# Optimization experiments

Measured on AMD Instinct MI355X. Metric: run time of the kernel, lower is better.

Reference implementation:

```python
import math
import jax, jax.numpy as jnp
import numpy as np

B = 2
N = 48           # max_atoms
A = 16           # num_atom_types
E = 5            # num_bond_types
HID = 384
NH = 8
HD = HID // NH   # 48
LYR = 4
MLP = 4 * HID
L = N + N * N    # 2352 sequence length (nodes + flattened edges)


def setup_inputs() -> dict:
    key = jax.random.key(0)
    ks = iter(jax.random.split(key, 48))
    r = lambda *s: jax.random.normal(next(ks), s, jnp.float32) * 0.02
    d = {
        "x": jax.random.normal(next(ks), (B, N, A), jnp.float32),
        "adj": jax.random.normal(next(ks), (B, N, N, E), jnp.float32),
        "t": jax.random.uniform(next(ks), (B,), jnp.float32),
        # embeddings
        "node_w": r(A, HID), "node_b": jnp.zeros((HID,), jnp.float32),
        "edge_w": r(E, HID), "edge_b": jnp.zeros((HID,), jnp.float32),
        "pos": r(L, HID),
        # timestep MLP (SinusoidalPositionalEmbedding(HID) -> Linear(HID,4H) -> SiLU -> Linear(4H,H))
        "t_w1": r(HID, 4 * HID), "t_b1": jnp.zeros((4 * HID,), jnp.float32),
        "t_w2": r(4 * HID, HID), "t_b2": jnp.zeros((HID,), jnp.float32),
        # stacked per-layer params
        "ada1_w": r(LYR, HID, 2 * HID), "ada1_b": jnp.zeros((LYR, 2 * HID), jnp.float32),
        "ada2_w": r(LYR, HID, 2 * HID), "ada2_b": jnp.zeros((LYR, 2 * HID), jnp.float32),
        "q_w": r(LYR, HID, HID), "q_b": jnp.zeros((LYR, HID), jnp.float32),
        "k_w": r(LYR, HID, HID), "k_b": jnp.zeros((LYR, HID), jnp.float32),
        "v_w": r(LYR, HID, HID), "v_b": jnp.zeros((LYR, HID), jnp.float32),
        "o_w": r(LYR, HID, HID), "o_b": jnp.zeros((LYR, HID), jnp.float32),
        "m1_w": r(LYR, HID, MLP), "m1_b": jnp.zeros((LYR, MLP), jnp.float32),
        "m2_w": r(LYR, MLP, HID), "m2_b": jnp.zeros((LYR, HID), jnp.float32),
        # final norm + heads (heads random instead of zero-init so output is informative)
        "fn_g": jnp.ones((HID,), jnp.float32), "fn_b": jnp.zeros((HID,), jnp.float32),
        "on_w": r(HID, A), "on_b": jnp.zeros((A,), jnp.float32),
        "oe_w": r(HID, E), "oe_b": jnp.zeros((E,), jnp.float32),
    }
    return d


def _ln(z):
    # LayerNorm(elementwise_affine=False), eps=1e-5
    mu = z.mean(-1, keepdims=True)
    var = z.var(-1, keepdims=True)
    return (z - mu) * jax.lax.rsqrt(var + 1e-5)


def _forward(x, adj, t, node_w, node_b, edge_w, edge_b, pos,
             t_w1, t_b1, t_w2, t_b2,
             ada1_w, ada1_b, ada2_w, ada2_b,
             q_w, q_b, k_w, k_b, v_w, v_b, o_w, o_b,
             m1_w, m1_b, m2_w, m2_b,
             fn_g, fn_b, on_w, on_b, oe_w, oe_b):
    b = x.shape[0]
    # embed nodes and edges, concat into sequence [b, L, HID]
    h_nodes = x @ node_w + node_b                       # [b, N, H]
    h_edges = adj.reshape(b, N * N, E) @ edge_w + edge_b  # [b, N*N, H]
    h = jnp.concatenate([h_nodes, h_edges], axis=1) + pos[None]
    # sinusoidal timestep embedding -> cond [b, HID]
    half = HID // 2
    freqs = jnp.exp(-math.log(10000.0) * jnp.arange(half, dtype=jnp.float32) / half)
    ang = t[:, None].astype(jnp.float32) * freqs[None, :]
    temb = jnp.concatenate([jnp.sin(ang), jnp.cos(ang)], axis=-1)
    cond = jax.nn.silu(temb @ t_w1 + t_b1) @ t_w2 + t_b2
    inv_scale = 1.0 / math.sqrt(HD)
    for i in range(LYR):
        # AdaLN 1 + attention
        sc, sh = jnp.split(cond @ ada1_w[i] + ada1_b[i], 2, axis=-1)
        n = _ln(h) * (1.0 + sc[:, None, :]) + sh[:, None, :]
        q = (n @ q_w[i] + q_b[i]).reshape(b, L, NH, HD)
        k = (n @ k_w[i] + k_b[i]).reshape(b, L, NH, HD)
        v = (n @ v_w[i] + v_b[i]).reshape(b, L, NH, HD)
        scores = jnp.einsum('bqhd,bkhd->bhqk', q, k) * inv_scale
        attn = jax.nn.softmax(scores, axis=-1)
        ao = jnp.einsum('bhqk,bkhd->bqhd', attn, v).reshape(b, L, HID)
        h = h + ao @ o_w[i] + o_b[i]
        # AdaLN 2 + MLP (exact GELU as in nn.GELU default)
        sc2, sh2 = jnp.split(cond @ ada2_w[i] + ada2_b[i], 2, axis=-1)
        n2 = _ln(h) * (1.0 + sc2[:, None, :]) + sh2[:, None, :]
        h = h + jax.nn.gelu(n2 @ m1_w[i] + m1_b[i], approximate=False) @ m2_w[i] + m2_b[i]
    h = _ln(h) * fn_g + fn_b
    node_out = h[:, :N] @ on_w + on_b                   # [b, N, A]
    edge_out = (h[:, N:] @ oe_w + oe_b).reshape(b, N, N, E)
    return node_out, edge_out


def reference(x, adj, t, node_w, node_b, edge_w, edge_b, pos,
              t_w1, t_b1, t_w2, t_b2,
              ada1_w, ada1_b, ada2_w, ada2_b,
              q_w, q_b, k_w, k_b, v_w, v_b, o_w, o_b,
              m1_w, m1_b, m2_w, m2_b,
              fn_g, fn_b, on_w, on_b, oe_w, oe_b):
    return _forward(x, adj, t, node_w, node_b, edge_w, edge_b, pos,
                    t_w1, t_b1, t_w2, t_b2,
                    ada1_w, ada1_b, ada2_w, ada2_b,
                    q_w, q_b, k_w, k_b, v_w, v_b, o_w, o_b,
                    m1_w, m1_b, m2_w, m2_b,
                    fn_g, fn_b, on_w, on_b, oe_w, oe_b)
```

## Files before the change

### kernel.cpp

```cpp
#include <hip/hip_runtime.h>
#include <hip/hip_bf16.h>
#include <math.h>

typedef __hip_bfloat16 bf16;
typedef __attribute__((ext_vector_type(8))) short short8;
typedef __attribute__((ext_vector_type(4))) float f32x4;

#define B_ 2
#define N_ 48
#define A_ 16
#define E_ 5
#define HID 384
#define NHD 8
#define HD 48
#define LYR 4
#define MLPD 1536
#define L_ 2352
#define M_ 4704
#define VLP 2432
#define QSCALE 0.20823513f

#define WQ_  0LL
#define WK_  589824LL
#define WV_  1179648LL
#define WO_  1769472LL
#define WM1_ 2359296LL
#define WM2_ 4718592LL
#define WTOT 7077888
#define BQ_  0
#define BK_  1536
#define BV_  3072
#define BO_  4608
#define BM1_ 6144
#define BM2_ 12288
#define BTOT 13824

#define PO_E  ((size_t)16*2368*2*48)
#define PML_E ((size_t)16*2368*2*2)

#define GLOAD16(gp, lp) __builtin_amdgcn_global_load_lds( \
    (const __attribute__((address_space(1))) unsigned int*)(gp), \
    (__attribute__((address_space(3))) unsigned int*)(lp), 16, 0, 0)

static __device__ __forceinline__ float b2f(bf16 v) { return __bfloat162float(v); }
static __device__ __forceinline__ float us2f(unsigned short u) {
    return __uint_as_float(((unsigned)u) << 16);
}
static __device__ __forceinline__ unsigned short f2us(float f) {
    bf16 h = __float2bfloat16(f);
    return *reinterpret_cast<unsigned short*>(&h);
}
static __device__ __forceinline__ float exp2_raw(float x) {
    float r;
    asm("v_exp_f32 %0, %1" : "=v"(r) : "v"(x));
    return r;
}
static __device__ __forceinline__ float ldv(const float* p, size_t i) { return p[i]; }
static __device__ __forceinline__ float ldv(const bf16*  p, size_t i) { return b2f(p[i]); }
static __device__ __forceinline__ void  stv(float* p, size_t i, float v) { p[i] = v; }
static __device__ __forceinline__ void  stv(bf16*  p, size_t i, float v) { p[i] = __float2bfloat16(v); }
static __device__ __forceinline__ float4 ld4(const float* p, size_t i) {
    return *reinterpret_cast<const float4*>(p + i);
}
static __device__ __forceinline__ float4 ld4(const bf16* p, size_t i) {
    ushort4 u = *reinterpret_cast<const ushort4*>(p + i);
    return make_float4(us2f(u.x), us2f(u.y), us2f(u.z), us2f(u.w));
}

__global__ void k_detect(const void* w, int* flag) {
    if (threadIdx.x == 0 && blockIdx.x == 0) {
        const bf16* p = (const bf16*)w;
        int isf = 0;
        for (int i = 0; i < 256; ++i) {
            float v = fabsf(b2f(p[i]));
            if (!(v <= 1000.0f)) { isf = 1; break; }
        }
        *flag = isf;
    }
}

template <typename T>
static __device__ void prepw_body(
    const T* q_w, const T* k_w, const T* v_w, const T* o_w,
    const T* m1_w, const T* m2_w, bf16* wbt)
{
    __shared__ unsigned short Ts[64][72];
    const int z = blockIdx.y;
    const int kind = z >> 2, l = z & 3;
    const T* src; int K, N; long long dbase;
    switch (kind) {
        case 0: src = q_w;  K = 384;  N = 384;  dbase = WQ_;  break;
        case 1: src = k_w;  K = 384;  N = 384;  dbase = WK_;  break;
        case 2: src = v_w;  K = 384;  N = 384;  dbase = WV_;  break;
        case 3: src = o_w;  K = 384;  N = 384;  dbase = WO_;  break;
        case 4: src = m1_w; K = 384;  N = 1536; dbase = WM1_; break;
        default: src = m2_w; K = 1536; N = 384; dbase = WM2_; break;
    }
    const int Nt = N >> 6;
    const int tiles = (K >> 6) * Nt;
    if (blockIdx.x >= tiles) return;
    const int tk = blockIdx.x / Nt, tn = blockIdx.x % Nt;
    const int k0 = tk*64, n0 = tn*64;
    const size_t soff = (size_t)l * K * N;
    const size_t doff = (size_t)dbase + (size_t)l * K * N;
    const int tid = threadIdx.x;
    {
        const int kk = tid >> 2, nc = (tid & 3) * 16;
        #pragma unroll
        for (int j = 0; j < 16; ++j)
            Ts[kk][nc + j] = f2us(ldv(src, soff + (size_t)(k0 + kk)*N + n0 + nc + j));
    }
    __syncthreads();
    {
        const int nn = tid >> 2, kc = (tid & 3) * 16;
        unsigned short tmp[16];
        #pragma unroll
        for (int j = 0; j < 16; ++j) tmp[j] = Ts[kc + j][nn];
        unsigned short* dst = (unsigned short*)wbt + doff + (size_t)(n0 + nn)*K + k0 + kc;
        *reinterpret_cast<short8*>(dst)     = *reinterpret_cast<short8*>(&tmp[0]);
        *reinterpret_cast<short8*>(dst + 8) = *reinterpret_cast<short8*>(&tmp[8]);
    }
}

__global__ __launch_bounds__(256) void k_prepw(
    const void* q_w, const void* k_w, const void* v_w, const void* o_w,
    const void* m1_w, const void* m2_w, const int* __restrict__ fl, bf16* __restrict__ wbt)
{
    if (*fl) prepw_body<float>((const float*)q_w, (const float*)k_w, (const float*)v_w,
                               (const float*)o_w, (const float*)m1_w, (const float*)m2_w, wbt);
    else     prepw_body<bf16>((const bf16*)q_w, (const bf16*)k_w, (const bf16*)v_w,
                              (const bf16*)o_w, (const bf16*)m1_w, (const bf16*)m2_w, wbt);
}

template <typename T>
static __device__ void prepb_body(
    const T* q_b, const T* k_b, const T* v_b, const T* o_b,
    const T* m1_b, const T* m2_b, bf16* bb)
{
    for (int i = threadIdx.x; i < BTOT; i += 256) {
        float v;
        if      (i < BK_)  v = ldv(q_b,  i);
        else if (i < BV_)  v = ldv(k_b,  i - BK_);
        else if (i < BO_)  v = ldv(v_b,  i - BV_);
        else if (i < BM1_) v = ldv(o_b,  i - BO_);
        else if (i < BM2_) v = ldv(m1_b, i - BM1_);
        else               v = ldv(m2_b, i - BM2_);
        bb[i] = __float2bfloat16(v);
    }
}

__global__ __launch_bounds__(256) void k_prepb(
    const void* q_b, const void* k_b, const void* v_b, const void* o_b,
    const void* m1_b, const void* m2_b, const int* __restrict__ fl, bf16* __restrict__ bb)
{
    if (*fl) prepb_body<float>((const float*)q_b, (const float*)k_b, (const float*)v_b,
                               (const float*)o_b, (const float*)m1_b, (const float*)m2_b, bb);
    else     prepb_body<bf16>((const bf16*)q_b, (const bf16*)k_b, (const bf16*)v_b,
                              (const bf16*)o_b, (const bf16*)m1_b, (const bf16*)m2_b, bb);
}

template <typename T>
static __device__ void embed_body(
    const T* x, const T* adj, const T* node_w, const T* node_b,
    const T* edge_w, const T* edge_b, const T* pos, float* h)
{
    const int bl = blockIdx.x;
    const int b = bl / L_, l = bl % L_;
    const int c = threadIdx.x;
    float acc;
    if (l < N_) {
        acc = ldv(node_b, c);
        const size_t xr = (size_t)(b*N_ + l)*A_;
        #pragma unroll
        for (int a = 0; a < A_; ++a) acc += ldv(x, xr + a) * ldv(node_w, (size_t)a*HID + c);
    } else {
        const int e = l - N_;
        acc = ldv(edge_b, c);
        const size_t ar = ((size_t)b*N_*N_ + e)*E_;
        #pragma unroll
        for (int j = 0; j < E_; ++j) acc += ldv(adj, ar + j) * ldv(edge_w, (size_t)j*HID + c);
    }
    h[(size_t)bl*HID + c] = acc + ldv(pos, (size_t)l*HID + c);
}

__global__ __launch_bounds__(384) void k_embed(
    const void* x, const void* adj, const void* node_w, const void* node_b,
    const void* edge_w, const void* edge_b, const void* pos,
    const int* __restrict__ fl, float* __restrict__ h)
{
    if (*fl) embed_body<float>((const float*)x, (const float*)adj, (const float*)node_w,
                               (const float*)node_b, (const float*)edge_w, (const float*)edge_b,
                               (const float*)pos, h);
    else     embed_body<bf16>((const bf16*)x, (const bf16*)adj, (const bf16*)node_w,
                              (const bf16*)node_b, (const bf16*)edge_w, (const bf16*)edge_b,
                              (const bf16*)pos, h);
}

template <typename T>
static __device__ void cond1_body(const T* t, const T* t_w1, const T* t_b1, float* hid)
{
    __shared__ float temb[HID];
    __shared__ float red[4][64];
    const int b = blockIdx.x, jb = blockIdx.y, tid = threadIdx.x;
    const float tv = ldv(t, b);
    for (int c = tid; c < HID; c += 256) {
        int i = (c < 192) ? c : c - 192;
        float f = expf(-9.2103403719761836f * (float)i / 192.0f);
        float ang = tv * f;
        temb[c] = (c < 192) ? sinf(ang) : cosf(ang);
    }
    __syncthreads();
    const int ko = tid >> 6, jo = tid & 63;
    const int j = jb*64 + jo;
    float acc = 0.f;
    for (int i = ko*96; i < (ko + 1)*96; ++i)
        acc += temb[i] * ldv(t_w1, (size_t)i*4*HID + j);
    red[ko][jo] = acc;
    __syncthreads();
    if (ko == 0) {
        float a = red[0][jo] + red[1][jo] + red[2][jo] + red[3][jo] + ldv(t_b1, j);
        hid[(size_t)b*4*HID + j] = a / (1.0f + expf(-a));
    }
}

__global__ __launch_bounds__(256) void k_cond1(
    const void* t, const void* t_w1, const void* t_b1,
    const int* __restrict__ fl, float* __restrict__ hid)
{
    if (*fl) cond1_body<float>((const float*)t, (const float*)t_w1, (const float*)t_b1, hid);
    else     cond1_body<bf16>((const bf16*)t, (const bf16*)t_w1, (const bf16*)t_b1, hid);
}

template <typename T>
static __device__ void cond2_body(const T* t_w2, const T* t_b2, const float* hid, float* part)
{
    __shared__ float hs[128];
    const int b = blockIdx.x, ch = blockIdx.y, c = threadIdx.x;
    const int j0 = ch*128;
    if (c < 128) hs[c] = hid[(size_t)b*4*HID + j0 + c];
    __syncthreads();
    float acc = (ch == 0) ? ldv(t_b2, c) : 0.f;
    for (int jj = 0; jj < 128; ++jj)
        acc += hs[jj] * ldv(t_w2, (size_t)(j0 + jj)*HID + c);
    part[((size_t)b*12 + ch)*HID + c] = acc;
}

__global__ __launch_bounds__(384) void k_cond2(
    const void* t_w2, const void* t_b2, const int* __restrict__ fl,
    const float* __restrict__ hid, float* __restrict__ part)
{
    if (*fl) cond2_body<float>((const float*)t_w2, (const float*)t_b2, hid, part);
    else     cond2_body<bf16>((const bf16*)t_w2, (const bf16*)t_b2, hid, part);
}

template <typename T>
static __device__ void cond3_body(
    const T* ada1_w, const T* ada1_b, const T* ada2_w, const T* ada2_b,
    const float* part, float* ada_out)
{
    __shared__ float cs[HID];
    const int slot = blockIdx.x / 3, ob = blockIdx.x % 3, b = blockIdx.y;
    const int tid = threadIdx.x;
    for (int c = tid; c < HID; c += 256) {
        float s = 0.f;
        #pragma unroll
        for (int ch = 0; ch < 12; ++ch) s += part[((size_t)b*12 + ch)*HID + c];
        cs[c] = s;
    }
    __syncthreads();
    const int layer = slot >> 1, which = slot & 1;
    const int o = ob*256 + tid;
    const T* W  = which ? ada2_w : ada1_w;
    const T* Bi = which ? ada2_b : ada1_b;
    float acc = ldv(Bi, (size_t)layer*768 + o);
    const size_t wb = (size_t)layer*HID*768 + o;
    for (int c = 0; c < HID; ++c) acc += cs[c] * ldv(W, wb + (size_t)c*768);
    ada_out[((size_t)slot*B_ + b)*768 + o] = acc;
}

__global__ __launch_bounds__(256) void k_cond3(
    const void* ada1_w, const void* ada1_b, const void* ada2_w, const void* ada2_b,
    const int* __restrict__ fl, const float* __restrict__ part, float* __restrict__ ada_out)
{
    if (*fl) cond3_body<float>((const float*)ada1_w, (const float*)ada1_b,
                               (const float*)ada2_w, (const float*)ada2_b, part, ada_out);
    else     cond3_body<bf16>((const bf16*)ada1_w, (const bf16*)ada1_b,
                              (const bf16*)ada2_w, (const bf16*)ada2_b, part, ada_out);
}

__global__ __launch_bounds__(256) void k_adaln(
    const float* __restrict__ h, const float* __restrict__ ada,
    bf16* __restrict__ n, int slot)
{
    const int row  = blockIdx.x * 4 + (threadIdx.x >> 6);
    const int lane = threadIdx.x & 63;
    const int b = row / L_;
    const float* hr = h + (size_t)row*HID;
    float v[6]; float s = 0.f, ss = 0.f;
    #pragma unroll
    for (int j = 0; j < 6; ++j) { float t = hr[lane + j*64]; v[j] = t; s += t; ss += t*t; }
    #pragma unroll
    for (int off = 32; off; off >>= 1) { s += __shfl_xor(s, off); ss += __shfl_xor(ss, off); }
    const float mu = s * (1.0f/HID);
    const float rs = rsqrtf(fmaxf(ss * (1.0f/HID) - mu*mu, 0.0f) + 1e-5f);
    const float* ap = ada + ((size_t)slot*B_ + b)*768;
    bf16* nr = n + (size_t)row*HID;
    #pragma unroll
    for (int j = 0; j < 6; ++j) {
        int c = lane + j*64;
        nr[c] = __float2bfloat16((v[j] - mu)*rs*(1.0f + ap[c]) + ap[384 + c]);
    }
}

static __device__ __forceinline__ void gemm_epilogue(
    f32x4 (&acc)[2][2], float bcol0, float bcol1,
    bf16* Cb, float* Cf, int M, int N, int act, int mode,
    int bm, int bn, int wm, int wn, int quad, int c)
{
    const float bcol[2] = {bcol0, bcol1};
    #pragma unroll
    for (int mi = 0; mi < 2; ++mi)
        #pragma unroll
        for (int ni = 0; ni < 2; ++ni) {
            const int col = bn + wn*32 + ni*16 + c;
            #pragma unroll
            for (int r = 0; r < 4; ++r) {
                const int row = bm + wm*32 + mi*16 + quad*4 + r;
                if (row < M) {
                    float v = acc[mi][ni][r] + bcol[ni];
                    if (act) v = 0.5f * v * (1.0f + erff(v * 0.70710678118654752f));
                    if (mode == 1) Cf[(size_t)row*N + col] += v;
                    else if (mode == 0) Cb[(size_t)row*N + col] = __float2bfloat16(v);
                    else if (mode == 3) Cb[(size_t)row*N + col] = __float2bfloat16(v * QSCALE);
                    else {
                        const int b   = row >= L_ ? 1 : 0;
                        const int key = row - b*L_;
                        const int hh  = col / 48, d = col - hh*48;
                        Cb[((size_t)(b*8 + hh)*48 + d)*VLP + key] = __float2bfloat16(v);
                    }
                }
            }
        }
}

template <typename T>
static __device__ void gemm_body(
    const bf16* A, const T* W, long long woff, const T* bias, long long boff,
    bf16* Cb, float* Cf, int M, int N, int K, int act, int mode)
{
    __shared__ __align__(16) unsigned short As[64][72];
    __shared__ __align__(16) unsigned short Bt[64][72];
    const int tid  = threadIdx.x;
    const int wv   = tid >> 6, lane = tid & 63;
    const int quad = lane >> 4, c = lane & 15;
    const int wm = wv & 1, wn = wv >> 1;
    const int bm = blockIdx.x * 64, bn = blockIdx.y * 64;
    const int arow = tid >> 3, ach = tid & 7;
    f32x4 acc[2][2] = {{{0.f,0.f,0.f,0.f},{0.f,0.f,0.f,0.f}},
                       {{0.f,0.f,0.f,0.f},{0.f,0.f,0.f,0.f}}};
    for (int k0 = 0; k0 < K; k0 += 64) {
        short8 av[2]; float4 w0[2], w1[2];
        #pragma unroll
        for (int i = 0; i < 2; ++i) {
            const int row = i*32 + arow;
            av[i] = short8{0,0,0,0,0,0,0,0};
            if (bm + row < M)
                av[i] = *reinterpret_cast<const short8*>(
                            A + (size_t)(bm + row)*K + k0 + ach*8);
            const size_t wrow = (size_t)woff + (size_t)(k0 + i*32 + arow)*N + bn + ach*8;
            w0[i] = ld4(W, wrow);
            w1[i] = ld4(W, wrow + 4);
        }
        __syncthreads();
        #pragma unroll
        for (int i = 0; i < 2; ++i) {
            *reinterpret_cast<short8*>(&As[i*32 + arow][ach*8]) = av[i];
            const int kk = i*32 + arow, nb0 = ach*8;
            Bt[nb0+0][kk] = f2us(w0[i].x); Bt[nb0+1][kk] = f2us(w0[i].y);
            Bt[nb0+2][kk] = f2us(w0[i].z); Bt[nb0+3][kk] = f2us(w0[i].w);
            Bt[nb0+4][kk] = f2us(w1[i].x); Bt[nb0+5][kk] = f2us(w1[i].y);
            Bt[nb0+6][kk] = f2us(w1[i].z); Bt[nb0+7][kk] = f2us(w1[i].w);
        }
        __syncthreads();
        #pragma unroll
        for (int ks = 0; ks < 2; ++ks) {
            short8 af[2], bfr[2];
            #pragma unroll
            for (int mi = 0; mi < 2; ++mi)
                af[mi] = *reinterpret_cast<const short8*>(
                             &As[wm*32 + mi*16 + c][ks*32 + quad*8]);
            #pragma unroll
            for (int ni = 0; ni < 2; ++ni)
                bfr[ni] = *reinterpret_cast<const short8*>(
                              &Bt[wn*32 + ni*16 + c][ks*32 + quad*8]);
            #pragma unroll
            for (int mi = 0; mi < 2; ++mi)
                #pragma unroll
                for (int ni = 0; ni < 2; ++ni)
                    acc[mi][ni] = __builtin_amdgcn_mfma_f32_16x16x32_bf16(
                                      af[mi], bfr[ni], acc[mi][ni], 0, 0, 0);
        }
    }
    gemm_epilogue(acc, ldv(bias, (size_t)boff + bn + wn*32 + c),
                  ldv(bias, (size_t)boff + bn + wn*32 + 16 + c),
                  Cb, Cf, M, N, act, mode, bm, bn, wm, wn, quad, c);
}

__global__ __launch_bounds__(256) void k_gemm(
    const bf16* __restrict__ A, const void* W, long long woff, const void* bias, long long boff,
    bf16* Cb, float* Cf, int M, int N, int K, int act, int mode,
    const int* __restrict__ fl)
{
    if (*fl) gemm_body<float>(A, (const float*)W, woff, (const float*)bias, boff,
                              Cb, Cf, M, N, K, act, mode);
    else     gemm_body<bf16>(A, (const bf16*)W, woff, (const bf16*)bias, boff,
                             Cb, Cf, M, N, K, act, mode);
}

__global__ __launch_bounds__(256) void k_gemm_qkv(
    const bf16* __restrict__ A,
    const void* qw, const void* kw, const void* vw,
    const void* qb, const void* kb, const void* vb,
    long long woff, long long boff,
    bf16* Cq, bf16* Ck, bf16* Cv, const int* __restrict__ fl)
{
    const int z = blockIdx.z;
    const void* W  = (z == 0) ? qw : (z == 1) ? kw : vw;
    const void* Bi = (z == 0) ? qb : (z == 1) ? kb : vb;
    bf16* C        = (z == 0) ? Cq : (z == 1) ? Ck : Cv;
    const int mode = (z == 0) ? 3 : (z == 2) ? 2 : 0;
    if (*fl) gemm_body<float>(A, (const float*)W, woff, (const float*)Bi, boff,
                              C, nullptr, M_, HID, HID, 0, mode);
    else     gemm_body<bf16>(A, (const bf16*)W, woff, (const bf16*)Bi, boff,
                             C, nullptr, M_, HID, HID, 0, mode);
}

static __device__ void gemm_t_body(
    const bf16* A, const bf16* Wt, long long woff, const bf16* bias, long long boff,
    bf16* Cb, float* Cf, int M, int N, int K, int act, int mode)
{
    __shared__ __align__(16) unsigned short Tz[2][2][4096];
    const int tid  = threadIdx.x;
    const int wv   = tid >> 6, lane = tid & 63;
    const int quad = lane >> 4, c = lane & 15;
    const int wm = wv & 1, wn = wv >> 1;
    const int bm = blockIdx.x * 64, bn = blockIdx.y * 64;
    const unsigned short* Ag = (const unsigned short*)A;
    const unsigned short* Wg = (const unsigned short*)Wt + woff;
    const int sr = tid >> 3;
    const int csw0 = (((tid & 7) ^ (sr & 7)) << 3);
    int ar0 = bm + sr;        ar0 = ar0 < M ? ar0 : M - 1;
    int ar1 = bm + 32 + sr;   ar1 = ar1 < M ? ar1 : M - 1;
    const int wr0 = bn + sr, wr1 = bn + 32 + sr;
    const int ldso = tid * 8;

    f32x4 acc[2][2] = {{{0.f,0.f,0.f,0.f},{0.f,0.f,0.f,0.f}},
                       {{0.f,0.f,0.f,0.f},{0.f,0.f,0.f,0.f}}};

    #define STAGE_T(buf, k0) do { \
        GLOAD16(Ag + (size_t)ar0*K + (k0) + csw0, &Tz[buf][0][ldso]); \
        GLOAD16(Ag + (size_t)ar1*K + (k0) + csw0, &Tz[buf][0][2048 + ldso]); \
        GLOAD16(Wg + (size_t)wr0*K + (k0) + csw0, &Tz[buf][1][ldso]); \
        GLOAD16(Wg + (size_t)wr1*K + (k0) + csw0, &Tz[buf][1][2048 + ldso]); \
    } while (0)

    STAGE_T(0, 0);
    __syncthreads();
    int cur = 0;
    for (int k0 = 0; k0 < K; k0 += 64) {
        if (k0 + 64 < K) STAGE_T(cur ^ 1, k0 + 64);
        #pragma unroll
        for (int ks = 0; ks < 2; ++ks) {
            short8 af[2], bfr[2];
            #pragma unroll
            for (int mi = 0; mi < 2; ++mi) {
                const int row = wm*32 + mi*16 + c;
                const char* p = (const char*)&Tz[cur][0][0]
                              + (row*128 + (((ks*64 + quad*16)) ^ ((row & 7) << 4)));
                af[mi] = *reinterpret_cast<const short8*>(p);
            }
            #pragma unroll
            for (int ni = 0; ni < 2; ++ni) {
                const int row = wn*32 + ni*16 + c;
                const char* p = (const char*)&Tz[cur][1][0]
                              + (row*128 + (((ks*64 + quad*16)) ^ ((row & 7) << 4)));
                bfr[ni] = *reinterpret_cast<const short8*>(p);
            }
            #pragma unroll
            for (int mi = 0; mi < 2; ++mi)
                #pragma unroll
                for (int ni = 0; ni < 2; ++ni)
                    acc[mi][ni] = __builtin_amdgcn_mfma_f32_16x16x32_bf16(
                                      af[mi], bfr[ni], acc[mi][ni], 0, 0, 0);
        }
        __syncthreads();
        cur ^= 1;
    }
    #undef STAGE_T
    gemm_epilogue(acc, b2f(bias[boff + bn + wn*32 + c]),
                  b2f(bias[boff + bn + wn*32 + 16 + c]),
                  Cb, Cf, M, N, act, mode, bm, bn, wm, wn, quad, c);
}

__global__ __launch_bounds__(256) void k_gemm_t(
    const bf16* __restrict__ A, const bf16* __restrict__ Wt, long long woff,
    const bf16* __restrict__ bias, long long boff,
    bf16* Cb, float* Cf, int M, int N, int K, int act, int mode)
{
    gemm_t_body(A, Wt, woff, bias, boff, Cb, Cf, M, N, K, act, mode);
}

__global__ __launch_bounds__(256) void k_gemm_qkv_t(
    const bf16* __restrict__ A, const bf16* __restrict__ wbt, const bf16* __restrict__ bb,
    int lyr, bf16* Cq, bf16* Ck, bf16* Cv)
{
    const int z = blockIdx.z;
    long long woff; long long boff; bf16* C; int mode;
    if (z == 0)      { woff = WQ_ + (long long)lyr*147456; boff = BQ_ + lyr*384; C = Cq; mode = 3; }
    else if (z == 1) { woff = WK_ + (long long)lyr*147456; boff = BK_ + lyr*384; C = Ck; mode = 0; }
    else             { woff = WV_ + (long long)lyr*147456; boff = BV_ + lyr*384; C = Cv; mode = 2; }
    gemm_t_body(A, wbt, woff, bb, boff, C, nullptr, M_, HID, HID, 0, mode);
}

__global__ __launch_bounds__(512) void k_attn(
    const bf16* __restrict__ q, const bf16* __restrict__ k,
    const bf16* __restrict__ vt, bf16* __restrict__ ao)
{
    __shared__ __align__(16) unsigned short Ks[2][64][80];
    __shared__ __align__(16) unsigned short Vt[2][48][72];
    __shared__ __align__(16) unsigned short Pq[8][16][72];
    const int tid  = threadIdx.x;
    const int w    = tid >> 6, lane = tid & 63;
    const int quad = lane >> 4, c = lane & 15;
    const int qt = w & 3, sp = w >> 2;
    const int bh = blockIdx.y;
    const size_t base  = (size_t)(bh >> 3)*L_*HID + (size_t)(bh & 7)*HD;
    const size_t vbase = (size_t)bh*48*VLP;
    const int q0 = blockIdx.x*64 + qt*16;
    const bool qvalid = q0 < L_;
    const int qrow = qvalid ? (q0 + c) : c;

    short8 qf0, qf1;
    {
        const unsigned short* qp = (const unsigned short*)(q + base + (size_t)qrow*HID);
        qf0 = *reinterpret_cast<const short8*>(qp + quad*8);
        if (quad < 2) qf1 = *reinterpret_cast<const short8*>(qp + 32 + quad*8);
        else          qf1 = short8{0,0,0,0,0,0,0,0};
    }
    f32x4 o0 = {0.f,0.f,0.f,0.f}, o1 = {0.f,0.f,0.f,0.f}, o2 = {0.f,0.f,0.f,0.f};
    float m = -3.0e38f, lsum = 0.f;

    const int t256 = tid & 255, grp = tid >> 8;
    const int krow0 = t256 >> 3, kch = t256 & 7;
    const int krow1 = 32 + krow0;
    const int vd0 = krow0;
    const int vd1 = 32 + (krow0 & 15);
    const bool vl1 = (t256 < 128);
    const unsigned short* kq = (const unsigned short*)(k + base);
    const unsigned short* vq = (const unsigned short*)(vt + vbase);
    const short8 Z8 = short8{0,0,0,0,0,0,0,0};
    short8 kr0 = Z8, kr1 = Z8, vr0, vr1 = Z8;
    {
        const int kb0 = grp*1216;
        if (kch < 6) {
            kr0 = *reinterpret_cast<const short8*>(kq + (size_t)(kb0 + krow0)*HID + kch*8);
            kr1 = *reinterpret_cast<const short8*>(kq + (size_t)(kb0 + krow1)*HID + kch*8);
        }
        vr0 = *reinterpret_cast<const short8*>(vq + (size_t)vd0*VLP + kb0 + kch*8);
        if (vl1) vr1 = *reinterpret_cast<const short8*>(vq + (size_t)vd1*VLP + kb0 + kch*8);
    }

    for (int tt = 0; tt < 19; ++tt) {
        __syncthreads();
        *reinterpret_cast<short8*>(&Ks[grp][krow0][kch*8]) = kr0;
        *reinterpret_cast<short8*>(&Ks[grp][krow1][kch*8]) = kr1;
        *reinterpret_cast<short8*>(&Vt[grp][vd0][kch*8])   = vr0;
        if (vl1) *reinterpret_cast<short8*>(&Vt[grp][vd1][kch*8]) = vr1;
        __syncthreads();
        if (tt < 18) {
            const int nb0 = grp*1216 + (tt + 1)*64;
            if (kch < 6) {
                kr0 = *reinterpret_cast<const short8*>(kq + (size_t)(nb0 + krow0)*HID + kch*8);
                kr1 = *reinterpret_cast<const short8*>(kq + (size_t)(nb0 + krow1)*HID + kch*8);
            }
            vr0 = *reinterpret_cast<const short8*>(vq + (size_t)vd0*VLP + nb0 + kch*8);
            if (vl1) vr1 = *reinterpret_cast<const short8*>(vq + (size_t)vd1*VLP + nb0 + kch*8);
        }

        const int kt = sp*1216 + tt*64;
        float sv[16];
        #pragma unroll
        for (int t = 0; t < 4; ++t) {
            f32x4 acc = {0.f,0.f,0.f,0.f};
            short8 a0 = *reinterpret_cast<const short8*>(&Ks[sp][t*16 + c][quad*8]);
            short8 a1 = *reinterpret_cast<const short8*>(&Ks[sp][t*16 + c][32 + quad*8]);
            acc = __builtin_amdgcn_mfma_f32_16x16x32_bf16(a0, qf0, acc, 0, 0, 0);
            acc = __builtin_amdgcn_mfma_f32_16x16x32_bf16(a1, qf1, acc, 0, 0, 0);
            #pragma unroll
            for (int r = 0; r < 4; ++r) sv[t*4 + r] = acc[r];
        }
        if (sp == 1 && tt >= 17) {
            #pragma unroll
            for (int t = 0; t < 4; ++t)
                #pragma unroll
                for (int r = 0; r < 4; ++r)
                    if (kt + t*16 + quad*4 + r >= L_) sv[t*4 + r] = -3.0e38f;
        }
        float tmax = fmaxf(fmaxf(fmaxf(sv[0], sv[1]),  fmaxf(sv[2],  sv[3])),
                           fmaxf(fmaxf(sv[4], sv[5]),  fmaxf(sv[6],  sv[7])));
        float tmx2 = fmaxf(fmaxf(fmaxf(sv[8], sv[9]),  fmaxf(sv[10], sv[11])),
                           fmaxf(fmaxf(sv[12], sv[13]), fmaxf(sv[14], sv[15])));
        tmax = fmaxf(tmax, tmx2);
        tmax = fmaxf(tmax, __shfl_xor(tmax, 16));
        tmax = fmaxf(tmax, __shfl_xor(tmax, 32));
        if (!__all(tmax <= m + 8.0f)) {
            const float mn = fmaxf(m, tmax);
            const float alpha = exp2f(m - mn);
            m = mn;
            lsum *= alpha;
            o0 *= alpha; o1 *= alpha; o2 *= alpha;
        }
        float psum = 0.f;
        unsigned short pv[16];
        #pragma unroll
        for (int i = 0; i < 16; ++i) {
            const float p = exp2f(sv[i] - m);
            psum += p;
            pv[i] = f2us(p);
        }
        lsum += psum;
        #pragma unroll
        for (int t = 0; t < 4; ++t)
            *reinterpret_cast<ushort4*>(&Pq[w][c][t*16 + quad*4]) =
                make_ushort4(pv[t*4+0], pv[t*4+1], pv[t*4+2], pv[t*4+3]);
        #pragma unroll
        for (int s = 0; s < 2; ++s) {
            short8 pf  = *reinterpret_cast<const short8*>(&Pq[w][c][s*32 + quad*8]);
            short8 vf0 = *reinterpret_cast<const short8*>(&Vt[sp][c][s*32 + quad*8]);
            short8 vf1 = *reinterpret_cast<const short8*>(&Vt[sp][16 + c][s*32 + quad*8]);
            short8 vf2 = *reinterpret_cast<const short8*>(&Vt[sp][32 + c][s*32 + quad*8]);
            o0 = __builtin_amdgcn_mfma_f32_16x16x32_bf16(vf0, pf, o0, 0, 0, 0);
            o1 = __builtin_amdgcn_mfma_f32_16x16x32_bf16(vf1, pf, o1, 0, 0, 0);
            o2 = __builtin_amdgcn_mfma_f32_16x16x32_bf16(vf2, pf, o2, 0, 0, 0);
        }
    }
    float lw = lsum;
    lw += __shfl_xor(lw, 16);
    lw += __shfl_xor(lw, 32);
    float* Mg = (float*)&Ks[0][0][0];
    __syncthreads();
    if (sp == 1) {
        float* dst = Mg + (size_t)(qt*64 + lane)*14;
        dst[0] = o0[0]; dst[1] = o0[1]; dst[2]  = o0[2]; dst[3]  = o0[3];
        dst[4] = o1[0]; dst[5] = o1[1]; dst[6]  = o1[2]; dst[7]  = o1[3];
        dst[8] = o2[0]; dst[9] = o2[1]; dst[10] = o2[2]; dst[11] = o2[3];
        dst[12] = m; dst[13] = lw;
    }
    __syncthreads();
    if (sp == 0 && qvalid) {
        const float* src = Mg + (size_t)(qt*64 + lane)*14;
        const float m2 = src[12], l2 = src[13];
        const float mm = fmaxf(m, m2);
        const float a1 = exp2f(m - mm), a2 = exp2f(m2 - mm);
        const float inv = 1.0f / (lw*a1 + l2*a2);
        unsigned short* orow = (unsigned short*)(ao + base + (size_t)(q0 + c)*HID);
        const f32x4 ot[3] = {o0, o1, o2};
        #pragma unroll
        for (int dt = 0; dt < 3; ++dt) {
            ushort4 w4;
            w4.x = f2us((ot[dt][0]*a1 + src[dt*4+0]*a2) * inv);
            w4.y = f2us((ot[dt][1]*a1 + src[dt*4+1]*a2) * inv);
            w4.z = f2us((ot[dt][2]*a1 + src[dt*4+2]*a2) * inv);
            w4.w = f2us((ot[dt][3]*a1 + src[dt*4+3]*a2) * inv);
            *reinterpret_cast<ushort4*>(orow + dt*16 + quad*4) = w4;
        }
    }
}

__global__ __launch_bounds__(256) void k_attn_fd(
    const bf16* __restrict__ q, const bf16* __restrict__ k,
    const bf16* __restrict__ vt, bf16* __restrict__ pob, float* __restrict__ pml)
{
    __shared__ __align__(16) unsigned short Ks[64][80];
    __shared__ __align__(16) unsigned short Vt[48][72];
    __shared__ __align__(16) unsigned short Pq[4][16][72];
    const int tid  = threadIdx.x;
    const int w    = tid >> 6, lane = tid & 63;
    const int quad = lane >> 4, c = lane & 15;
    const int bh   = blockIdx.y;
    const int half = blockIdx.z;
    const size_t base  = (size_t)(bh >> 3)*L_*HID + (size_t)(bh & 7)*HD;
    const size_t vbase = (size_t)bh*48*VLP;
    const int q0 = blockIdx.x*64 + w*16;
    const bool qvalid = q0 < L_;
    const int qrow = qvalid ? (q0 + c) : c;

    short8 qf0, qf1;
    {
        const unsigned short* qp = (const unsigned short*)(q + base + (size_t)qrow*HID);
        qf0 = *reinterpret_cast<const short8*>(qp + quad*8);
        if (quad < 2) qf1 = *reinterpret_cast<const short8*>(qp + 32 + quad*8);
        else          qf1 = short8{0,0,0,0,0,0,0,0};
    }
    f32x4 o0 = {0.f,0.f,0.f,0.f}, o1 = {0.f,0.f,0.f,0.f}, o2 = {0.f,0.f,0.f,0.f};
    float m = -3.0e38f, lsum = 0.f;

    const int krow0 = tid >> 3, kch = tid & 7;
    const int krow1 = 32 + krow0;
    const int vd0 = krow0;
    const int vd1 = 32 + (krow0 & 15);
    const bool vl1 = (tid < 128);
    const unsigned short* kq = (const unsigned short*)(k + base);
    const unsigned short* vq = (const unsigned short*)(vt + vbase);
    const short8 Z8 = short8{0,0,0,0,0,0,0,0};
    short8 kr0 = Z8, kr1 = Z8, vr0, vr1 = Z8;
    const int kbase = half*1216;
    {
        if (kch < 6) {
            kr0 = *reinterpret_cast<const short8*>(kq + (size_t)(kbase + krow0)*HID + kch*8);
            kr1 = *reinterpret_cast<const short8*>(kq + (size_t)(kbase + krow1)*HID + kch*8);
        }
        vr0 = *reinterpret_cast<const short8*>(vq + (size_t)vd0*VLP + kbase + kch*8);
        if (vl1) vr1 = *reinterpret_cast<const short8*>(vq + (size_t)vd1*VLP + kbase + kch*8);
    }

    for (int tt = 0; tt < 19; ++tt) {
        __syncthreads();
        *reinterpret_cast<short8*>(&Ks[krow0][kch*8]) = kr0;
        *reinterpret_cast<short8*>(&Ks[krow1][kch*8]) = kr1;
        *reinterpret_cast<short8*>(&Vt[vd0][kch*8])   = vr0;
        if (vl1) *reinterpret_cast<short8*>(&Vt[vd1][kch*8]) = vr1;
        __syncthreads();
        if (tt < 18) {
            const int nb0 = kbase + (tt + 1)*64;
            if (kch < 6) {
                kr0 = *reinterpret_cast<const short8*>(kq + (size_t)(nb0 + krow0)*HID + kch*8);
                kr1 = *reinterpret_cast<const short8*>(kq + (size_t)(nb0 + krow1)*HID + kch*8);
            }
            vr0 = *reinterpret_cast<const short8*>(vq + (size_t)vd0*VLP + nb0 + kch*8);
            if (vl1) vr1 = *reinterpret_cast<const short8*>(vq + (size_t)vd1*VLP + nb0 + kch*8);
        }

        const int kt = kbase + tt*64;
        float sv[16];
        #pragma unroll
        for (int t = 0; t < 4; ++t) {
            f32x4 acc = {0.f,0.f,0.f,0.f};
            short8 a0 = *reinterpret_cast<const short8*>(&Ks[t*16 + c][quad*8]);
            short8 a1 = *reinterpret_cast<const short8*>(&Ks[t*16 + c][32 + quad*8]);
            acc = __builtin_amdgcn_mfma_f32_16x16x32_bf16(a0, qf0, acc, 0, 0, 0);
            acc = __builtin_amdgcn_mfma_f32_16x16x32_bf16(a1, qf1, acc, 0, 0, 0);
            #pragma unroll
            for (int r = 0; r < 4; ++r) sv[t*4 + r] = acc[r];
        }
        if (half == 1 && tt >= 17) {
            #pragma unroll
            for (int t = 0; t < 4; ++t)
                #pragma unroll
                for (int r = 0; r < 4; ++r)
                    if (kt + t*16 + quad*4 + r >= L_) sv[t*4 + r] = -3.0e38f;
        }
        float h0 = fmaxf(fmaxf(sv[0], sv[1]), sv[2]);
        h0 = fmaxf(fmaxf(h0, sv[3]), sv[4]);
        h0 = fmaxf(fmaxf(h0, sv[5]), sv[6]);
        h0 = fmaxf(h0, sv[7]);
        float h1 = fmaxf(fmaxf(sv[8], sv[9]), sv[10]);
        h1 = fmaxf(fmaxf(h1, sv[11]), sv[12]);
        h1 = fmaxf(fmaxf(h1, sv[13]), sv[14]);
        h1 = fmaxf(h1, sv[15]);
        float tmax = fmaxf(h0, h1);
        tmax = fmaxf(tmax, __shfl_xor(tmax, 16));
        tmax = fmaxf(tmax, __shfl_xor(tmax, 32));
        if (!__all(tmax <= m + 8.0f)) {
            const float mn = fmaxf(m, tmax);
            const float alpha = exp2_raw(m - mn);
            m = mn;
            lsum *= alpha;
            o0 *= alpha; o1 *= alpha; o2 *= alpha;
        }
        float psum = 0.f;
        unsigned pk[8];
        #pragma unroll
        for (int i = 0; i < 8; ++i) {
            const float p0 = exp2_raw(sv[2*i]     - m);
            const float p1 = exp2_raw(sv[2*i + 1] - m);
            psum += p0 + p1;
            pk[i] = (__float_as_uint(p0) >> 16) | (__float_as_uint(p1) & 0xFFFF0000u);
        }
        lsum += psum;
        #pragma unroll
        for (int t = 0; t < 4; ++t)
            *reinterpret_cast<uint2*>(&Pq[w][c][t*16 + quad*4]) =
                make_uint2(pk[2*t], pk[2*t + 1]);
        #pragma unroll
        for (int s = 0; s < 2; ++s) {
            short8 pf  = *reinterpret_cast<const short8*>(&Pq[w][c][s*32 + quad*8]);
            short8 vf0 = *reinterpret_cast<const short8*>(&Vt[c][s*32 + quad*8]);
            short8 vf1 = *reinterpret_cast<const short8*>(&Vt[16 + c][s*32 + quad*8]);
            short8 vf2 = *reinterpret_cast<const short8*>(&Vt[32 + c][s*32 + quad*8]);
            o0 = __builtin_amdgcn_mfma_f32_16x16x32_bf16(vf0, pf, o0, 0, 0, 0);
            o1 = __builtin_amdgcn_mfma_f32_16x16x32_bf16(vf1, pf, o1, 0, 0, 0);
            o2 = __builtin_amdgcn_mfma_f32_16x16x32_bf16(vf2, pf, o2, 0, 0, 0);
        }
    }
    float lw = lsum;
    lw += __shfl_xor(lw, 16);
    lw += __shfl_xor(lw, 32);
    const float invl = 1.0f / lw;
    const size_t ro = ((size_t)bh*2368 + q0 + c)*2 + half;
    unsigned short* pr = (unsigned short*)pob + ro*48;
    const f32x4 ot[3] = {o0, o1, o2};
    #pragma unroll
    for (int dt = 0; dt < 3; ++dt) {
        ushort4 w4;
        w4.x = f2us(ot[dt][0]*invl);
        w4.y = f2us(ot[dt][1]*invl);
        w4.z = f2us(ot[dt][2]*invl);
        w4.w = f2us(ot[dt][3]*invl);
        *reinterpret_cast<ushort4*>(pr + dt*16 + quad*4) = w4;
    }
    if (quad == 0) { pml[ro*2 + 0] = m; pml[ro*2 + 1] = lw; }
}

__global__ __launch_bounds__(256) void k_amerge(
    const bf16* __restrict__ pob, const float* __restrict__ pml, bf16* __restrict__ ao)
{
    const int tid = threadIdx.x;
    const int bh = blockIdx.y;
    const int qq = blockIdx.x*16 + (tid >> 4);
    const int j = tid & 15;
    const size_t ro = ((size_t)bh*2368 + qq)*2;
    const float m1 = pml[ro*2 + 0], l1 = pml[ro*2 + 1];
    const float m2 = pml[ro*2 + 2], l2 = pml[ro*2 + 3];
    const float mm = fmaxf(m1, m2);
    const float b1 = exp2f(m1 - mm)*l1, b2 = exp2f(m2 - mm)*l2;
    const float inv = 1.0f / (b1 + b2);
    const float w1 = b1*inv, w2 = b2*inv;
    if (j < 12) {
        const unsigned short* p1 = (const unsigned short*)pob + ro*48 + j*4;
        ushort4 u1 = *reinterpret_cast<const ushort4*>(p1);
        ushort4 u2 = *reinterpret_cast<const ushort4*>(p1 + 48);
        ushort4 o4;
        o4.x = f2us(us2f(u1.x)*w1 + us2f(u2.x)*w2);
        o4.y = f2us(us2f(u1.y)*w1 + us2f(u2.y)*w2);
        o4.z = f2us(us2f(u1.z)*w1 + us2f(u2.z)*w2);
        o4.w = f2us(us2f(u1.w)*w1 + us2f(u2.w)*w2);
        const size_t base = (size_t)(bh >> 3)*L_*HID + (size_t)(bh & 7)*HD;
        *reinterpret_cast<ushort4*>((unsigned short*)ao + base + (size_t)qq*HID + j*4) = o4;
    }
}

template <typename T, typename TO>
static __device__ void final_body(
    const float* h, const T* fn_g, const T* fn_b,
    const T* on_w, const T* on_b, const T* oe_w, const T* oe_b, TO* out)
{
    __shared__ float hf[HID];
    const int row = blockIdx.x;
    const int b = row / L_, l = row % L_;
    const int lane = threadIdx.x;
    const float* hr = h + (size_t)row*HID;
    float v[6]; float s = 0.f, ss = 0.f;
    #pragma unroll
    for (int j = 0; j < 6; ++j) { float t = hr[lane + j*64]; v[j] = t; s += t; ss += t*t; }
    #pragma unroll
    for (int off = 32; off; off >>= 1) { s += __shfl_xor(s, off); ss += __shfl_xor(ss, off); }
    const float mu = s * (1.0f/HID);
    const float rs = rsqrtf(fmaxf(ss * (1.0f/HID) - mu*mu, 0.0f) + 1e-5f);
    #pragma unroll
    for (int j = 0; j < 6; ++j) {
        int c = lane + j*64;
        hf[c] = (v[j] - mu) * rs * ldv(fn_g, c) + ldv(fn_b, c);
    }
    __syncthreads();
    if (l < N_) {
        if (lane < A_) {
            float acc = ldv(on_b, lane);
            for (int c = 0; c < HID; ++c) acc += hf[c] * ldv(on_w, (size_t)c*A_ + lane);
            stv(out, (size_t)(b*N_ + l)*A_ + lane, acc);
        }
    } else {
        const int e = l - N_;
        if (lane < E_) {
            float acc = ldv(oe_b, lane);
            for (int c = 0; c < HID; ++c) acc += hf[c] * ldv(oe_w, (size_t)c*E_ + lane);
            stv(out, (size_t)B_*N_*A_ + ((size_t)b*N_*N_ + e)*E_ + lane, acc);
        }
    }
}

__global__ __launch_bounds__(64) void k_final(
    const float* __restrict__ h, const void* fn_g, const void* fn_b,
    const void* on_w, const void* on_b, const void* oe_w, const void* oe_b,
    const int* __restrict__ fl, void* out)
{
    if (*fl) final_body<float, float>(h, (const float*)fn_g, (const float*)fn_b,
                                      (const float*)on_w, (const float*)on_b,
                                      (const float*)oe_w, (const float*)oe_b, (float*)out);
    else     final_body<bf16, bf16>(h, (const bf16*)fn_g, (const bf16*)fn_b,
                                    (const bf16*)on_w, (const bf16*)on_b,
                                    (const bf16*)oe_w, (const bf16*)oe_b, (bf16*)out);
}

extern "C" void kernel_launch(void* const* d_in, const int* in_sizes, int n_in,
                              void* d_out, int out_size, void* d_ws, size_t ws_size,
                              hipStream_t stream) {
    const void* x      = d_in[0];
    const void* adj    = d_in[1];
    const void* t      = d_in[2];
    const void* node_w = d_in[3];
    const void* node_b = d_in[4];
    const void* edge_w = d_in[5];
    const void* edge_b = d_in[6];
    const void* pos    = d_in[7];
    const void* t_w1   = d_in[8];
    const void* t_b1   = d_in[9];
    const void* t_w2   = d_in[10];
    const void* t_b2   = d_in[11];
    const void* ada1_w = d_in[12];
    const void* ada1_b = d_in[13];
    const void* ada2_w = d_in[14];
    const void* ada2_b = d_in[15];
    const void* q_w    = d_in[16];
    const void* q_b    = d_in[17];
    const void* k_w    = d_in[18];
    const void* k_b    = d_in[19];
    const void* v_w    = d_in[20];
    const void* v_b    = d_in[21];
    const void* o_w    = d_in[22];
    const void* o_b    = d_in[23];
    const void* m1_w   = d_in[24];
    const void* m1_b   = d_in[25];
    const void* m2_w   = d_in[26];
    const void* m2_b   = d_in[27];
    const void* fn_g   = d_in[28];
    const void* fn_b   = d_in[29];
    const void* on_w   = d_in[30];
    const void* on_b   = d_in[31];
    const void* oe_w   = d_in[32];
    const void* oe_b   = d_in[33];

    const size_t SZ  = (size_t)M_ * HID;
    const size_t VTZ = (size_t)B_*NHD*HD*VLP;
    const size_t FLT = SZ + 12288 + (size_t)B_*4*HID + (size_t)B_*12*HID;
    const size_t M1FULL = (size_t)M_ * MLPD;
    const size_t BF_BASE = 3*SZ + VTZ;
    const size_t BF_BIG  = SZ + M1FULL;
    const size_t NEED      = 256 + sizeof(float)*FLT + sizeof(bf16)*BF_BASE;
    const size_t NEED_BIG  = 256 + sizeof(float)*FLT + sizeof(bf16)*BF_BIG;
    const size_t NEED_PREP = 256 + sizeof(float)*FLT
                           + sizeof(bf16)*(BF_BIG + WTOT + BTOT);
    const size_t NEED_FD   = NEED_PREP + sizeof(bf16)*PO_E + sizeof(float)*PML_E;
    if (ws_size < NEED) {
        hipMemsetAsync(d_out, 0, (size_t)out_size*sizeof(bf16), stream);
        return;
    }
    const bool big  = (ws_size >= NEED_BIG);
    const bool prep = (ws_size >= NEED_PREP);
    const bool fd   = (ws_size >= NEED_FD);
    int*   fl   = (int*)d_ws;
    float* h    = (float*)((char*)d_ws + 256);
    float* ada  = h + SZ;
    float* hid  = ada + 12288;
    float* part = hid + (size_t)B_*4*HID;
    bf16* nb  = (bf16*)(part + (size_t)B_*12*HID);
    bf16* qb  = nb + SZ;
    bf16* kb  = qb + SZ;
    bf16* vtb = kb + SZ;
    bf16* m1c = kb;
    bf16* m1f = qb;
    bf16* wbt = nb + BF_BIG;
    bf16* bb  = wbt + WTOT;
    bf16* pob = bb + BTOT;
    float* pml = (float*)(pob + PO_E);

    k_detect<<<1, 64, 0, stream>>>(node_w, fl);
    if (prep) {
        k_prepw<<<dim3(144, 24), 256, 0, stream>>>(q_w, k_w, v_w, o_w, m1_w, m2_w, fl, wbt);
        k_prepb<<<1, 256, 0, stream>>>(q_b, k_b, v_b, o_b, m1_b, m2_b, fl, bb);
    }
    k_embed<<<M_, HID, 0, stream>>>(x, adj, node_w, node_b, edge_w, edge_b, pos, fl, h);
    k_cond1<<<dim3(B_, 24), 256, 0, stream>>>(t, t_w1, t_b1, fl, hid);
    k_cond2<<<dim3(B_, 12), 384, 0, stream>>>(t_w2, t_b2, fl, hid, part);
    k_cond3<<<dim3(24, B_), 256, 0, stream>>>(ada1_w, ada1_b, ada2_w, ada2_b, fl, part, ada);
    for (int i = 0; i < LYR; ++i) {
        const long long woff   = (long long)i * HID * HID;
        const long long boff   = (long long)i * HID;
        const long long m1woff = (long long)i * HID * MLPD;
        const long long m1boff = (long long)i * MLPD;
        const long long m2woff = (long long)i * MLPD * HID;

        k_adaln<<<M_/4, 256, 0, stream>>>(h, ada, nb, 2*i);
        if (prep) {
            k_gemm_qkv_t<<<dim3(74, 6, 3), 256, 0, stream>>>(nb, wbt, bb, i, qb, kb, vtb);
            if (fd) {
                k_attn_fd<<<dim3(37, 16, 2), 256, 0, stream>>>(qb, kb, vtb, pob, pml);
                k_amerge<<<dim3(147, 16), 256, 0, stream>>>(pob, pml, nb);
            } else {
                k_attn<<<dim3(37, B_*NHD), 512, 0, stream>>>(qb, kb, vtb, nb);
            }
            k_gemm_t<<<dim3(74, 6), 256, 0, stream>>>(nb, wbt, WO_ + (long long)i*147456,
                                                      bb, BO_ + i*384,
                                                      nullptr, h, M_, HID, HID, 0, 1);
            k_adaln<<<M_/4, 256, 0, stream>>>(h, ada, nb, 2*i + 1);
            k_gemm_t<<<dim3(74, 24), 256, 0, stream>>>(nb, wbt, WM1_ + (long long)i*589824,
                                                       bb, BM1_ + i*MLPD,
                                                       m1f, nullptr, M_, MLPD, HID, 1, 0);
            k_gemm_t<<<dim3(74, 6), 256, 0, stream>>>(m1f, wbt, WM2_ + (long long)i*589824,
                                                      bb, BM2_ + i*384,
                                                      nullptr, h, M_, HID, MLPD, 0, 1);
        } else {
            k_gemm_qkv<<<dim3(74, 6, 3), 256, 0, stream>>>(nb, q_w, k_w, v_w, q_b, k_b, v_b,
                                                           woff, boff, qb, kb, vtb, fl);
            k_attn<<<dim3(37, B_*NHD), 512, 0, stream>>>(qb, kb, vtb, nb);
            k_gemm<<<dim3(74, 6), 256, 0, stream>>>(nb, o_w, woff, o_b, boff,
                                                    nullptr, h, M_, HID, HID, 0, 1, fl);
            k_adaln<<<M_/4, 256, 0, stream>>>(h, ada, nb, 2*i + 1);
            if (big) {
                k_gemm<<<dim3(74, 24), 256, 0, stream>>>(nb, m1_w, m1woff, m1_b, m1boff,
                                                         m1f, nullptr, M_, MLPD, HID, 1, 0, fl);
                k_gemm<<<dim3(74, 6), 256, 0, stream>>>(m1f, m2_w, m2woff, m2_b, boff,
                                                        nullptr, h, M_, HID, MLPD, 0, 1, fl);
            } else {
                for (int c = 0; c < 2; ++c) {
                    k_gemm<<<dim3(37, 24), 256, 0, stream>>>(nb + (size_t)c*2352*HID,
                                                             m1_w, m1woff, m1_b, m1boff,
                                                             m1c, nullptr, 2352, MLPD, HID, 1, 0, fl);
                    k_gemm<<<dim3(37, 6), 256, 0, stream>>>(m1c, m2_w, m2woff, m2_b, boff,
                                                            nullptr, h + (size_t)c*2352*HID,
                                                            2352, HID, MLPD, 0, 1, fl);
                }
            }
        }
    }
    k_final<<<M_, 64, 0, stream>>>(h, fn_g, fn_b, on_w, on_b, oe_w, oe_b, fl, (void*)d_out);
}
```

Baseline: 771.6 us.

## Double-buffer split-KV attention tiles with direct global-to-LDS loads and XOR swizzle

Replaces register-staged K/V tile loads in the split-KV attention kernel with direct global-to-LDS copies (GLOAD16) into two ping-pong LDS buffers. The LDS layout drops the padded rows for an XOR-swizzled 64-element row, which is meant to avoid bank conflicts. Padding columns are zeroed once. This cuts one barrier per iteration and register traffic, and lets the next tile's loads overlap compute. In exchange it uses more LDS, which may lower occupancy, and it depends on GLOAD16 completing before the trailing barrier.

```diff
diff --git a/kernel.cpp b/kernel.cpp
--- a/kernel.cpp
+++ b/kernel.cpp
@@ -681,8 +681,8 @@
     const bf16* __restrict__ q, const bf16* __restrict__ k,
     const bf16* __restrict__ vt, bf16* __restrict__ pob, float* __restrict__ pml)
 {
-    __shared__ __align__(16) unsigned short Ks[64][80];
-    __shared__ __align__(16) unsigned short Vt[48][72];
+    __shared__ __align__(16) unsigned short Kz[2][4096];
+    __shared__ __align__(16) unsigned short Vz[2][3072];
     __shared__ __align__(16) unsigned short Pq[4][16][72];
     const int tid  = threadIdx.x;
     const int w    = tid >> 6, lane = tid & 63;
@@ -705,49 +705,54 @@
     f32x4 o0 = {0.f,0.f,0.f,0.f}, o1 = {0.f,0.f,0.f,0.f}, o2 = {0.f,0.f,0.f,0.f};
     float m = -3.0e38f, lsum = 0.f;
 
-    const int krow0 = tid >> 3, kch = tid & 7;
-    const int krow1 = 32 + krow0;
-    const int vd0 = krow0;
-    const int vd1 = 32 + (krow0 & 15);
-    const bool vl1 = (tid < 128);
+    const int srow = tid >> 3;
+    const int sc   = (tid & 7) ^ (srow & 7);
+    const int scol = sc << 3;
+    const bool kld = (sc < 6);
+    const int ldo  = tid * 8;
     const unsigned short* kq = (const unsigned short*)(k + base);
     const unsigned short* vq = (const unsigned short*)(vt + vbase);
-    const short8 Z8 = short8{0,0,0,0,0,0,0,0};
-    short8 kr0 = Z8, kr1 = Z8, vr0, vr1 = Z8;
     const int kbase = half*1216;
+
+    #define STAGE_FD(buf, kb) do { \
+        if (kld) { \
+            GLOAD16(kq + (size_t)((kb) + srow)*HID + scol,      &Kz[buf][ldo]); \
+            GLOAD16(kq + (size_t)((kb) + 32 + srow)*HID + scol, &Kz[buf][2048 + ldo]); \
+        } \
+        GLOAD16(vq + (size_t)srow*VLP + (kb) + scol, &Vz[buf][ldo]); \
+        if (tid < 128) \
+            GLOAD16(vq + (size_t)(32 + srow)*VLP + (kb) + scol, &Vz[buf][2048 + ldo]); \
+    } while (0)
+
     {
-        if (kch < 6) {
-            kr0 = *reinterpret_cast<const short8*>(kq + (size_t)(kbase + krow0)*HID + kch*8);
-            kr1 = *reinterpret_cast<const short8*>(kq + (size_t)(kbase + krow1)*HID + kch*8);
-        }
-        vr0 = *reinterpret_cast<const short8*>(vq + (size_t)vd0*VLP + kbase + kch*8);
-        if (vl1) vr1 = *reinterpret_cast<const short8*>(vq + (size_t)vd1*VLP + kbase + kch*8);
-    }
+        const short8 Z8 = short8{0,0,0,0,0,0,0,0};
+        if (tid < 128) {
+            const int r = tid >> 1, j = tid & 1;
+            const int s = (6 + j) ^ (r & 7);
+            *reinterpret_cast<short8*>(&Kz[0][r*64 + s*8]) = Z8;
+            *reinterpret_cast<short8*>(&Kz[1][r*64 + s*8]) = Z8;
+        }
+    }
+    STAGE_FD(0, kbase);
+    __syncthreads();
+    int cur = 0;
 
     for (int tt = 0; tt < 19; ++tt) {
-        __syncthreads();
-        *reinterpret_cast<short8*>(&Ks[krow0][kch*8]) = kr0;
-        *reinterpret_cast<short8*>(&Ks[krow1][kch*8]) = kr1;
-        *reinterpret_cast<short8*>(&Vt[vd0][kch*8])   = vr0;
-        if (vl1) *reinterpret_cast<short8*>(&Vt[vd1][kch*8]) = vr1;
-        __syncthreads();
-        if (tt < 18) {
-            const int nb0 = kbase + (tt + 1)*64;
-            if (kch < 6) {
-                kr0 = *reinterpret_cast<const short8*>(kq + (size_t)(nb0 + krow0)*HID + kch*8);
-                kr1 = *reinterpret_cast<const short8*>(kq + (size_t)(nb0 + krow1)*HID + kch*8);
-            }
-            vr0 = *reinterpret_cast<const short8*>(vq + (size_t)vd0*VLP + nb0 + kch*8);
-            if (vl1) vr1 = *reinterpret_cast<const short8*>(vq + (size_t)vd1*VLP + nb0 + kch*8);
-        }
+        if (tt < 18) STAGE_FD(cur ^ 1, kbase + (tt + 1)*64);
 
         const int kt = kbase + tt*64;
+        const char* kzb = (const char*)&Kz[cur][0];
+        const char* vzb = (const char*)&Vz[cur][0];
+        const int qx = quad << 4;
         float sv[16];
         #pragma unroll
         for (int t = 0; t < 4; ++t) {
+            const int kr = t*16 + c;
+            const int rx = kr*128;
+            const int x0 = qx ^ ((kr & 7) << 4);
             f32x4 acc = {0.f,0.f,0.f,0.f};
-            short8 a0 = *reinterpret_cast<const short8*>(&Ks[t*16 + c][quad*8]);
-            short8 a1 = *reinterpret_cast<const short8*>(&Ks[t*16 + c][32 + quad*8]);
+            short8 a0 = *reinterpret_cast<const short8*>(kzb + rx + x0);
+            short8 a1 = *reinterpret_cast<const short8*>(kzb + rx + (x0 ^ 64));
             acc = __builtin_amdgcn_mfma_f32_16x16x32_bf16(a0, qf0, acc, 0, 0, 0);
             acc = __builtin_amdgcn_mfma_f32_16x16x32_bf16(a1, qf1, acc, 0, 0, 0);
             #pragma unroll
@@ -792,17 +797,22 @@
         for (int t = 0; t < 4; ++t)
             *reinterpret_cast<uint2*>(&Pq[w][c][t*16 + quad*4]) =
                 make_uint2(pk[2*t], pk[2*t + 1]);
+        const int mx = (c & 7) << 4;
         #pragma unroll
         for (int s = 0; s < 2; ++s) {
+            const int va = ((s << 6) | qx) ^ mx;
             short8 pf  = *reinterpret_cast<const short8*>(&Pq[w][c][s*32 + quad*8]);
-            short8 vf0 = *reinterpret_cast<const short8*>(&Vt[c][s*32 + quad*8]);
-            short8 vf1 = *reinterpret_cast<const short8*>(&Vt[16 + c][s*32 + quad*8]);
-            short8 vf2 = *reinterpret_cast<const short8*>(&Vt[32 + c][s*32 + quad*8]);
+            short8 vf0 = *reinterpret_cast<const short8*>(vzb + c*128 + va);
+            short8 vf1 = *reinterpret_cast<const short8*>(vzb + (16 + c)*128 + va);
+            short8 vf2 = *reinterpret_cast<const short8*>(vzb + (32 + c)*128 + va);
             o0 = __builtin_amdgcn_mfma_f32_16x16x32_bf16(vf0, pf, o0, 0, 0, 0);
             o1 = __builtin_amdgcn_mfma_f32_16x16x32_bf16(vf1, pf, o1, 0, 0, 0);
             o2 = __builtin_amdgcn_mfma_f32_16x16x32_bf16(vf2, pf, o2, 0, 0, 0);
         }
-    }
+        __syncthreads();
+        cur ^= 1;
+    }
+    #undef STAGE_FD
     float lw = lsum;
     lw += __shfl_xor(lw, 16);
     lw += __shfl_xor(lw, 32);
```

After: 779.8 us. About the same (+1.1%).
